# Kernel tuning notes

Measured on AMD Instinct MI355X. Metric: run time of the kernel, lower is better.

The kernel has to match this reference:

```python
import jax, jax.numpy as jnp
import numpy as np

N_NODES = 100000
N_EDGES = 600000
IN_DIM = 128
HID = 128
OUT_DIM = 64
N_LAYERS = 3


def setup_inputs() -> dict:
    key = jax.random.key(0)
    ks = jax.random.split(key, 8)
    x = jax.random.normal(ks[0], (N_NODES, IN_DIM), dtype=jnp.float32)
    edge_index = jax.random.randint(ks[1], (2, N_EDGES), 0, N_NODES, dtype=jnp.int64)
    s = 1.0 / np.sqrt(HID)
    W_in = jax.random.normal(ks[2], (HID, IN_DIM), dtype=jnp.float32) * s
    b_in = jax.random.normal(ks[3], (HID,), dtype=jnp.float32) * s
    W_convs = jax.random.normal(ks[4], (N_LAYERS, HID, HID), dtype=jnp.float32) * s
    b_convs = jax.random.normal(ks[5], (N_LAYERS, HID), dtype=jnp.float32) * s
    W_out = jax.random.normal(ks[6], (OUT_DIM, (N_LAYERS + 1) * HID), dtype=jnp.float32) * s
    b_out = jax.random.normal(ks[7], (OUT_DIM,), dtype=jnp.float32) * s
    return {"x": x, "edge_index": edge_index, "W_in": W_in, "b_in": b_in,
            "W_convs": W_convs, "b_convs": b_convs, "W_out": W_out, "b_out": b_out}


def reference(x, edge_index, W_in, b_in, W_convs, b_convs, W_out, b_out):
    src, dst = edge_index[0], edge_index[1]
    n = x.shape[0]
    # input projection: [N, in] -> [N, H]
    h = x @ W_in.T + b_in
    hidden_states = [h]
    for i in range(W_convs.shape[0]):
        # GINConv (eps=0): nn(x + sum of neighbor messages), messages src->dst
        agg = jax.ops.segment_sum(h[src], dst, num_segments=n)
        h = (h + agg) @ W_convs[i].T + b_convs[i]
        hidden_states.append(h)
    cat = jnp.concatenate(hidden_states, axis=1)  # [N, (L+1)*H]
    out = cat @ W_out.T + b_out  # [N, OUT]
    return jax.nn.softmax(out, axis=-1)
```

## Files before the change

### kernel.cpp

```cpp
#include <hip/hip_runtime.h>
#include <hip/hip_bf16.h>
#include <hip/hip_fp16.h>

#define GN 100000
#define GE 600000
#define SCAN_NBLK 98
#define ALD 132

typedef __bf16    bf16x8 __attribute__((ext_vector_type(8)));
typedef __bf16    bf16x4 __attribute__((ext_vector_type(4)));
typedef _Float16  f16x8  __attribute__((ext_vector_type(8)));
typedef float     f32x4  __attribute__((ext_vector_type(4)));

__global__ __launch_bounds__(256) void convert_w(
    const float* __restrict__ Win, const float* __restrict__ Wc,
    const float* __restrict__ Wout,
    __bf16* __restrict__ hi, __bf16* __restrict__ lo)
{
    const int i = blockIdx.x * 256 + threadIdx.x;
    if (i >= 98304) return;
    float v;
    if (i < 16384)      v = Win[i];
    else if (i < 65536) v = Wc[i - 16384];
    else                v = Wout[i - 65536];
    const __bf16 h = (__bf16)v;
    hi[i] = h;
    lo[i] = (__bf16)(v - (float)h);
}

__device__ __forceinline__ void gather8_f16(
    const uint* __restrict__ Hw,
    const int* __restrict__ row_start,
    const int* __restrict__ deg,
    const int* __restrict__ csr,
    const int row0, const int wave, const int lane,
    float* __restrict__ Acc)
{
    float2 acc8[8];
    int start8[8], deg8[8];
    int maxd = 0;
#pragma unroll
    for (int r = 0; r < 8; ++r) {
        acc8[r] = make_float2(0.f, 0.f);
        const int v = row0 + wave * 8 + r;
        start8[r] = row_start[v];
        deg8[r]   = deg[v];
        maxd = max(maxd, deg8[r]);
    }

    for (int b = 0; b < maxd; b += 64) {
        int idx8[8];
#pragma unroll
        for (int r = 0; r < 8; ++r) {
            const int off = max(min(b + lane, deg8[r] - 1), 0);
            idx8[r] = min(max(csr[start8[r] + off], 0), GN - 1);
        }
        const int wend = min(maxd - b, 64);
        for (int c = 0; c < wend; c += 8) {
            uint t[8][8];
#pragma unroll
            for (int cc = 0; cc < 8; ++cc)
#pragma unroll
                for (int r = 0; r < 8; ++r)
                    t[cc][r] = Hw[(size_t)__shfl(idx8[r], c + cc) * 64 + lane];
#pragma unroll
            for (int cc = 0; cc < 8; ++cc) {
                const int k = b + c + cc;
#pragma unroll
                for (int r = 0; r < 8; ++r) {
                    union { uint u; _Float16 h[2]; } cv;
                    cv.u = (k < deg8[r]) ? t[cc][r] : 0u;
                    acc8[r].x += (float)cv.h[0];
                    acc8[r].y += (float)cv.h[1];
                }
            }
        }
    }

    const int j = lane * 2;
#pragma unroll
    for (int r = 0; r < 8; ++r) {
        float* a = &Acc[(wave * 8 + r) * ALD + j];
        a[0] += acc8[r].x;
        a[1] += acc8[r].y;
    }
}

template<bool GATHER>
__global__ __launch_bounds__(256, 3) void gin_layer(
    const float* __restrict__ H, int ldH,
    const _Float16* __restrict__ HfIn,
    const int* __restrict__ row_start,
    const int* __restrict__ deg,
    const int* __restrict__ csr,
    const __bf16* __restrict__ Whi,
    const __bf16* __restrict__ Wlo,
    const float* __restrict__ bias,
    float* __restrict__ C, int ldC,
    _Float16* __restrict__ HfOut)
{
    __shared__ float Acc[32 * ALD];

    const int tid  = threadIdx.x;
    const int wave = tid >> 6;
    const int lane = tid & 63;
    const int row0 = blockIdx.x * 32;
    const int wn   = wave * 32;
    const int quad = lane >> 4;
    const int l15  = lane & 15;

    {
        const int sr = wave * 8 + (lane >> 5) ;
        float4 sv[4];
#pragma unroll
        for (int p = 0; p < 4; ++p) {
            const int r = wave * 8 + p * 2 + (lane >> 5);
            sv[p] = *(const float4*)(H + (size_t)(row0 + r) * ldH + (lane & 31) * 4);
        }
#pragma unroll
        for (int p = 0; p < 4; ++p) {
            const int r = wave * 8 + p * 2 + (lane >> 5);
            *(float4*)&Acc[r * ALD + (lane & 31) * 4] = sv[p];
        }
        (void)sr;
    }
    if (GATHER)
        gather8_f16((const uint*)HfIn, row_start, deg, csr, row0, wave, lane, Acc);
    __syncthreads();

    f32x4 acc[2][2];
#pragma unroll
    for (int i = 0; i < 2; ++i)
#pragma unroll
        for (int j = 0; j < 2; ++j) acc[i][j] = (f32x4)(0.0f);

    bf16x8 whA[2], wlA[2], whB[2], wlB[2];
#pragma unroll
    for (int nt = 0; nt < 2; ++nt) {
        const int n = wn + nt * 16 + l15;
        whA[nt] = *(const bf16x8*)(Whi + (size_t)n * 128 + quad * 8);
        wlA[nt] = *(const bf16x8*)(Wlo + (size_t)n * 128 + quad * 8);
    }

#pragma unroll
    for (int ks = 0; ks < 4; ++ks) {
        const int kt = ks * 32 + quad * 8;
        if (ks < 3) {
            const int kn = kt + 32;
#pragma unroll
            for (int nt = 0; nt < 2; ++nt) {
                const int n = wn + nt * 16 + l15;
                whB[nt] = *(const bf16x8*)(Whi + (size_t)n * 128 + kn);
                wlB[nt] = *(const bf16x8*)(Wlo + (size_t)n * 128 + kn);
            }
        }
        bf16x8 ahi[2], alo[2];
#pragma unroll
        for (int mt = 0; mt < 2; ++mt) {
            const float* ap = &Acc[(mt * 16 + l15) * ALD + kt];
            const f32x4 p = *(const f32x4*)ap;
            const f32x4 q = *(const f32x4*)(ap + 4);
#pragma unroll
            for (int e = 0; e < 4; ++e) {
                const __bf16 hp = (__bf16)p[e];
                const __bf16 hq = (__bf16)q[e];
                ahi[mt][e]     = hp;
                ahi[mt][e + 4] = hq;
                alo[mt][e]     = (__bf16)(p[e] - (float)hp);
                alo[mt][e + 4] = (__bf16)(q[e] - (float)hq);
            }
        }
#pragma unroll
        for (int mt = 0; mt < 2; ++mt)
#pragma unroll
            for (int nt = 0; nt < 2; ++nt) {
                acc[mt][nt] = __builtin_amdgcn_mfma_f32_16x16x32_bf16(
                    ahi[mt], whA[nt], acc[mt][nt], 0, 0, 0);
                acc[mt][nt] = __builtin_amdgcn_mfma_f32_16x16x32_bf16(
                    ahi[mt], wlA[nt], acc[mt][nt], 0, 0, 0);
                acc[mt][nt] = __builtin_amdgcn_mfma_f32_16x16x32_bf16(
                    alo[mt], whA[nt], acc[mt][nt], 0, 0, 0);
            }
        if (ks < 3) {
#pragma unroll
            for (int nt = 0; nt < 2; ++nt) {
                whA[nt] = whB[nt];
                wlA[nt] = wlB[nt];
            }
        }
    }
    __syncthreads();

#pragma unroll
    for (int nt = 0; nt < 2; ++nt) {
        const int col = wn + nt * 16 + l15;
        const float b = bias[col];
#pragma unroll
        for (int mt = 0; mt < 2; ++mt)
#pragma unroll
            for (int r4 = 0; r4 < 4; ++r4)
                Acc[(mt * 16 + quad * 4 + r4) * ALD + col] = acc[mt][nt][r4] + b;
    }
    __syncthreads();
#pragma unroll
    for (int p = 0; p < 4; ++p) {
        const int q  = tid + p * 256;
        const int r  = q >> 5;
        const int c4 = (q & 31) * 4;
        *(float4*)(C + (size_t)(row0 + r) * ldC + c4) = *(const float4*)&Acc[r * ALD + c4];
    }
#pragma unroll
    for (int p = 0; p < 2; ++p) {
        const int q = tid + p * 256;
        const int r = q >> 4;
        const int g = (q & 15) * 8;
        const float4 a = *(const float4*)&Acc[r * ALD + g];
        const float4 b = *(const float4*)&Acc[r * ALD + g + 4];
        f16x8 o = {(_Float16)a.x, (_Float16)a.y, (_Float16)a.z, (_Float16)a.w,
                   (_Float16)b.x, (_Float16)b.y, (_Float16)b.z, (_Float16)b.w};
        *(f16x8*)&HfOut[(size_t)(row0 + r) * 128 + g] = o;
    }
}

__global__ __launch_bounds__(256, 3) void gin_final(
    const float* __restrict__ cat3,
    const _Float16* __restrict__ HfIn,
    const int* __restrict__ row_start,
    const int* __restrict__ deg,
    const int* __restrict__ csr,
    const __bf16* __restrict__ Whi3,
    const __bf16* __restrict__ Wlo3,
    const float* __restrict__ b3,
    const __bf16* __restrict__ WhiO,
    const __bf16* __restrict__ WloO,
    const float* __restrict__ bO,
    float* __restrict__ out)
{
    constexpr int CLD = 68;

    __shared__ float Smem[32 * ALD];
    float* const Acc = Smem;
    float* const Cst = Smem;

    const int tid  = threadIdx.x;
    const int wave = tid >> 6;
    const int lane = tid & 63;
    const int row0 = blockIdx.x * 32;
    const int quad = lane >> 4;
    const int l15  = lane & 15;

    {
        float4 sv[4];
#pragma unroll
        for (int p = 0; p < 4; ++p) {
            const int r = wave * 8 + p * 2 + (lane >> 5);
            sv[p] = *(const float4*)(cat3 + (size_t)(row0 + r) * 384 + 256 + (lane & 31) * 4);
        }
#pragma unroll
        for (int p = 0; p < 4; ++p) {
            const int r = wave * 8 + p * 2 + (lane >> 5);
            *(float4*)&Acc[r * ALD + (lane & 31) * 4] = sv[p];
        }
    }
    gather8_f16((const uint*)HfIn, row_start, deg, csr, row0, wave, lane, Acc);
    __syncthreads();

    const int wn = wave * 32;
    f32x4 acc1[2][2];
#pragma unroll
    for (int i = 0; i < 2; ++i)
#pragma unroll
        for (int j = 0; j < 2; ++j) acc1[i][j] = (f32x4)(0.0f);

    {
        bf16x8 whA[2], wlA[2], whB[2], wlB[2];
#pragma unroll
        for (int nt = 0; nt < 2; ++nt) {
            const int n = wn + nt * 16 + l15;
            whA[nt] = *(const bf16x8*)(Whi3 + (size_t)n * 128 + quad * 8);
            wlA[nt] = *(const bf16x8*)(Wlo3 + (size_t)n * 128 + quad * 8);
        }
#pragma unroll
        for (int ks = 0; ks < 4; ++ks) {
            const int kt = ks * 32 + quad * 8;
            if (ks < 3) {
                const int kn = kt + 32;
#pragma unroll
                for (int nt = 0; nt < 2; ++nt) {
                    const int n = wn + nt * 16 + l15;
                    whB[nt] = *(const bf16x8*)(Whi3 + (size_t)n * 128 + kn);
                    wlB[nt] = *(const bf16x8*)(Wlo3 + (size_t)n * 128 + kn);
                }
            }
            bf16x8 ahi[2], alo[2];
#pragma unroll
            for (int mt = 0; mt < 2; ++mt) {
                const float* ap = &Acc[(mt * 16 + l15) * ALD + kt];
                const f32x4 p = *(const f32x4*)ap;
                const f32x4 q = *(const f32x4*)(ap + 4);
#pragma unroll
                for (int e = 0; e < 4; ++e) {
                    const __bf16 hp = (__bf16)p[e];
                    const __bf16 hq = (__bf16)q[e];
                    ahi[mt][e]     = hp;
                    ahi[mt][e + 4] = hq;
                    alo[mt][e]     = (__bf16)(p[e] - (float)hp);
                    alo[mt][e + 4] = (__bf16)(q[e] - (float)hq);
                }
            }
#pragma unroll
            for (int mt = 0; mt < 2; ++mt)
#pragma unroll
                for (int nt = 0; nt < 2; ++nt) {
                    acc1[mt][nt] = __builtin_amdgcn_mfma_f32_16x16x32_bf16(
                        ahi[mt], whA[nt], acc1[mt][nt], 0, 0, 0);
                    acc1[mt][nt] = __builtin_amdgcn_mfma_f32_16x16x32_bf16(
                        ahi[mt], wlA[nt], acc1[mt][nt], 0, 0, 0);
                    acc1[mt][nt] = __builtin_amdgcn_mfma_f32_16x16x32_bf16(
                        alo[mt], whA[nt], acc1[mt][nt], 0, 0, 0);
                }
            if (ks < 3) {
#pragma unroll
                for (int nt = 0; nt < 2; ++nt) {
                    whA[nt] = whB[nt];
                    wlA[nt] = wlB[nt];
                }
            }
        }
    }
    __syncthreads();

#pragma unroll
    for (int nt = 0; nt < 2; ++nt) {
        const int col = wn + nt * 16 + l15;
        const float b = b3[col];
#pragma unroll
        for (int mt = 0; mt < 2; ++mt)
#pragma unroll
            for (int r4 = 0; r4 < 4; ++r4)
                Acc[(mt * 16 + quad * 4 + r4) * ALD + col] = acc1[mt][nt][r4] + b;
    }
    __syncthreads();

    const int wk  = wave & 1;
    const int wn2 = (wave >> 1) * 32;
    f32x4 acc2[2][2];
#pragma unroll
    for (int i = 0; i < 2; ++i)
#pragma unroll
        for (int j = 0; j < 2; ++j) acc2[i][j] = (f32x4)(0.0f);

    f32x4 pA[2], qA[2], pB[2], qB[2];
    bf16x8 whA[2], wlA[2], whB[2], wlB[2];

    {
        const int kg = wk * 256 + quad * 8;
#pragma unroll
        for (int mt = 0; mt < 2; ++mt) {
            const int row = mt * 16 + l15;
            const float* ap = cat3 + (size_t)(row0 + row) * 384 + kg;
            pA[mt] = *(const f32x4*)ap;
            qA[mt] = *(const f32x4*)(ap + 4);
        }
#pragma unroll
        for (int nt = 0; nt < 2; ++nt) {
            const int n = wn2 + nt * 16 + l15;
            whA[nt] = *(const bf16x8*)(WhiO + (size_t)n * 512 + kg);
            wlA[nt] = *(const bf16x8*)(WloO + (size_t)n * 512 + kg);
        }
    }

#pragma unroll
    for (int ks = 0; ks < 8; ++ks) {
        if (ks < 7) {
            const int kg = wk * 256 + (ks + 1) * 32 + quad * 8;
#pragma unroll
            for (int mt = 0; mt < 2; ++mt) {
                const int row = mt * 16 + l15;
                if (kg < 384) {
                    const float* ap = cat3 + (size_t)(row0 + row) * 384 + kg;
                    pB[mt] = *(const f32x4*)ap;
                    qB[mt] = *(const f32x4*)(ap + 4);
                } else {
                    const float* ap = &Acc[row * ALD + (kg - 384)];
                    pB[mt] = *(const f32x4*)ap;
                    qB[mt] = *(const f32x4*)(ap + 4);
                }
            }
#pragma unroll
            for (int nt = 0; nt < 2; ++nt) {
                const int n = wn2 + nt * 16 + l15;
                whB[nt] = *(const bf16x8*)(WhiO + (size_t)n * 512 + kg);
                wlB[nt] = *(const bf16x8*)(WloO + (size_t)n * 512 + kg);
            }
        }
        bf16x8 ahi[2], alo[2];
#pragma unroll
        for (int mt = 0; mt < 2; ++mt) {
#pragma unroll
            for (int e = 0; e < 4; ++e) {
                const __bf16 hp = (__bf16)pA[mt][e];
                const __bf16 hq = (__bf16)qA[mt][e];
                ahi[mt][e]     = hp;
                ahi[mt][e + 4] = hq;
                alo[mt][e]     = (__bf16)(pA[mt][e] - (float)hp);
                alo[mt][e + 4] = (__bf16)(qA[mt][e] - (float)hq);
            }
        }
#pragma unroll
        for (int mt = 0; mt < 2; ++mt)
#pragma unroll
            for (int nt = 0; nt < 2; ++nt) {
                acc2[mt][nt] = __builtin_amdgcn_mfma_f32_16x16x32_bf16(
                    ahi[mt], whA[nt], acc2[mt][nt], 0, 0, 0);
                acc2[mt][nt] = __builtin_amdgcn_mfma_f32_16x16x32_bf16(
                    ahi[mt], wlA[nt], acc2[mt][nt], 0, 0, 0);
                acc2[mt][nt] = __builtin_amdgcn_mfma_f32_16x16x32_bf16(
                    alo[mt], whA[nt], acc2[mt][nt], 0, 0, 0);
            }
        if (ks < 7) {
#pragma unroll
            for (int mt = 0; mt < 2; ++mt) { pA[mt] = pB[mt]; qA[mt] = qB[mt]; }
#pragma unroll
            for (int nt = 0; nt < 2; ++nt) { whA[nt] = whB[nt]; wlA[nt] = wlB[nt]; }
        }
    }

    __syncthreads();

    if (wk == 1) {
#pragma unroll
        for (int nt = 0; nt < 2; ++nt)
#pragma unroll
            for (int mt = 0; mt < 2; ++mt)
#pragma unroll
                for (int r4 = 0; r4 < 4; ++r4)
                    Cst[(mt * 16 + quad * 4 + r4) * CLD + wn2 + nt * 16 + l15]
                        = acc2[mt][nt][r4];
    }
    __syncthreads();
    if (wk == 0) {
#pragma unroll
        for (int nt = 0; nt < 2; ++nt) {
            const int col = wn2 + nt * 16 + l15;
            const float b = bO[col];
#pragma unroll
            for (int mt = 0; mt < 2; ++mt)
#pragma unroll
                for (int r4 = 0; r4 < 4; ++r4) {
                    const int idx = (mt * 16 + quad * 4 + r4) * CLD + col;
                    Cst[idx] = Cst[idx] + acc2[mt][nt][r4] + b;
                }
        }
    }
    __syncthreads();

    for (int i = 0; i < 8; ++i) {
        const int r = wave * 8 + i;
        const float v = Cst[r * CLD + lane];
        float m = v;
#pragma unroll
        for (int off = 32; off > 0; off >>= 1) m = fmaxf(m, __shfl_xor(m, off));
        const float e = __expf(v - m);
        float s = e;
#pragma unroll
        for (int off = 32; off > 0; off >>= 1) s += __shfl_xor(s, off);
        out[(size_t)(row0 + r) * 64 + lane] = e / s;
    }
}

__global__ __launch_bounds__(256) void count_deg(const int* __restrict__ dst,
                                                 int* __restrict__ deg)
{
    const int e = blockIdx.x * 256 + threadIdx.x;
    if (e < GE) atomicAdd(&deg[dst[e]], 1);
}

__global__ __launch_bounds__(256) void scan_pass1(const int* __restrict__ deg,
                                                  int* __restrict__ excl,
                                                  int* __restrict__ blockSums)
{
    __shared__ int s[256];
    const int t = threadIdx.x;
    const int base = blockIdx.x * 1024 + t * 4;

    int4 v = make_int4(0, 0, 0, 0);
    if (base + 3 < GN) {
        v = *(const int4*)(deg + base);
    } else {
        if (base + 0 < GN) v.x = deg[base + 0];
        if (base + 1 < GN) v.y = deg[base + 1];
        if (base + 2 < GN) v.z = deg[base + 2];
        if (base + 3 < GN) v.w = deg[base + 3];
    }
    const int mysum = v.x + v.y + v.z + v.w;
    s[t] = mysum;
    __syncthreads();
    for (int off = 1; off < 256; off <<= 1) {
        const int val = (t >= off) ? s[t - off] : 0;
        __syncthreads();
        s[t] += val;
        __syncthreads();
    }
    int4 o;
    o.x = s[t] - mysum;
    o.y = o.x + v.x;
    o.z = o.y + v.y;
    o.w = o.z + v.z;
    if (base + 3 < GN) {
        *(int4*)(excl + base) = o;
    } else {
        if (base + 0 < GN) excl[base + 0] = o.x;
        if (base + 1 < GN) excl[base + 1] = o.y;
        if (base + 2 < GN) excl[base + 2] = o.z;
        if (base + 3 < GN) excl[base + 3] = o.w;
    }
    if (t == 255) blockSums[blockIdx.x] = s[255];
}

__global__ __launch_bounds__(128) void scan_pass2(const int* __restrict__ blockSums,
                                                  int* __restrict__ blockOffs, int n)
{
    __shared__ int s[128];
    const int t = threadIdx.x;
    const int v = (t < n) ? blockSums[t] : 0;
    s[t] = v;
    __syncthreads();
    for (int off = 1; off < 128; off <<= 1) {
        const int val = (t >= off) ? s[t - off] : 0;
        __syncthreads();
        s[t] += val;
        __syncthreads();
    }
    if (t < n) blockOffs[t] = s[t] - v;
}

__global__ __launch_bounds__(256) void scan_pass3(int* __restrict__ excl,
                                                  const int* __restrict__ blockOffs,
                                                  int* __restrict__ cursor)
{
    const int i = blockIdx.x * 256 + threadIdx.x;
    if (i >= GN) return;
    const int v = excl[i] + blockOffs[i >> 10];
    excl[i]   = v;
    cursor[i] = v;
}

__global__ __launch_bounds__(256) void fill_csr(const int* __restrict__ src,
                                                const int* __restrict__ dst,
                                                int* __restrict__ cursor,
                                                int* __restrict__ csr)
{
    const int e = blockIdx.x * 256 + threadIdx.x;
    if (e >= GE) return;
    const int pos = atomicAdd(&cursor[dst[e]], 1);
    csr[pos] = src[e];
}

extern "C" void kernel_launch(void* const* d_in, const int* in_sizes, int n_in,
                              void* d_out, int out_size, void* d_ws, size_t ws_size,
                              hipStream_t stream)
{
    const float* x       = (const float*)d_in[0];
    const int*   src     = (const int*)d_in[1];
    const int*   dst     = ((const int*)d_in[1]) + GE;
    const float* W_in    = (const float*)d_in[2];
    const float* b_in    = (const float*)d_in[3];
    const float* W_convs = (const float*)d_in[4];
    const float* b_convs = (const float*)d_in[5];
    const float* W_out   = (const float*)d_in[6];
    const float* b_out   = (const float*)d_in[7];
    float*       out     = (float*)d_out;

    float*    cat3 = (float*)d_ws;
    _Float16* Hf0  = (_Float16*)(cat3 + (size_t)GN * 384);
    _Float16* Hf1  = Hf0 + (size_t)GN * 128;
    int*      deg       = (int*)(Hf1 + (size_t)GN * 128);
    int*      row_start = deg + GN;
    int*      cursor    = row_start + GN;
    int*      blockSums = cursor + GN;
    int*      blockOffs = blockSums + 128;
    int*      csr       = blockOffs + 128;
    __bf16*   Whi       = (__bf16*)(csr + GE);
    __bf16*   Wlo       = Whi + 98304;

    const dim3 blk(256);
    const dim3 gblk(256);
    const int edge_blocks  = (GE + 255) / 256;
    const int node_blocks  = (GN + 255) / 256;
    const int layer_blocks = GN / 32;

    hipMemsetAsync(deg, 0, GN * sizeof(int), stream);
    count_deg<<<edge_blocks, blk, 0, stream>>>(dst, deg);
    scan_pass1<<<SCAN_NBLK, blk, 0, stream>>>(deg, row_start, blockSums);
    scan_pass2<<<1, 128, 0, stream>>>(blockSums, blockOffs, SCAN_NBLK);
    scan_pass3<<<node_blocks, blk, 0, stream>>>(row_start, blockOffs, cursor);
    fill_csr<<<edge_blocks, blk, 0, stream>>>(src, dst, cursor, csr);

    convert_w<<<(98304 + 255) / 256, blk, 0, stream>>>(W_in, W_convs, W_out, Whi, Wlo);

    gin_layer<false><<<layer_blocks, gblk, 0, stream>>>(
        x, 128, nullptr, nullptr, nullptr, nullptr,
        Whi, Wlo, b_in, cat3, 384, Hf0);

    gin_layer<true><<<layer_blocks, gblk, 0, stream>>>(
        cat3, 384, Hf0, row_start, deg, csr,
        Whi + 16384, Wlo + 16384, b_convs, cat3 + 128, 384, Hf1);
    gin_layer<true><<<layer_blocks, gblk, 0, stream>>>(
        cat3 + 128, 384, Hf1, row_start, deg, csr,
        Whi + 32768, Wlo + 32768, b_convs + 128, cat3 + 256, 384, Hf0);

    gin_final<<<layer_blocks, gblk, 0, stream>>>(
        cat3, Hf0, row_start, deg, csr,
        Whi + 49152, Wlo + 49152, b_convs + 256,
        Whi + 65536, Wlo + 65536, b_out, out);
}
```

Measured before the change: 473.1 us.

## Split neighbor gather into a standalone per-row kernel writing fp32 aggregates

Moves the fused in-GEMM neighbor aggregation out into a separate gather kernel, with one wave per destination row and high occupancy. It writes a float32 aggregate buffer that the layer GEMM kernels add to H when staging into LDS. The aim is to stop the gather's latency-bound, register-heavy loop from limiting the GEMM kernel's occupancy, and to avoid padding every row in a wave to the group's maximum degree. The cost is three extra launches plus writing and re-reading a 51 MB fp32 buffer per layer.

```diff
diff --git a/kernel.cpp b/kernel.cpp
--- a/kernel.cpp
+++ b/kernel.cpp
@@ -28,71 +28,51 @@
     lo[i] = (__bf16)(v - (float)h);
 }
 
-__device__ __forceinline__ void gather8_f16(
+__global__ __launch_bounds__(256, 8) void gather_rows(
     const uint* __restrict__ Hw,
     const int* __restrict__ row_start,
     const int* __restrict__ deg,
     const int* __restrict__ csr,
-    const int row0, const int wave, const int lane,
-    float* __restrict__ Acc)
-{
-    float2 acc8[8];
-    int start8[8], deg8[8];
-    int maxd = 0;
-#pragma unroll
-    for (int r = 0; r < 8; ++r) {
-        acc8[r] = make_float2(0.f, 0.f);
-        const int v = row0 + wave * 8 + r;
-        start8[r] = row_start[v];
-        deg8[r]   = deg[v];
-        maxd = max(maxd, deg8[r]);
-    }
-
-    for (int b = 0; b < maxd; b += 64) {
-        int idx8[8];
-#pragma unroll
-        for (int r = 0; r < 8; ++r) {
-            const int off = max(min(b + lane, deg8[r] - 1), 0);
-            idx8[r] = min(max(csr[start8[r] + off], 0), GN - 1);
-        }
-        const int wend = min(maxd - b, 64);
-        for (int c = 0; c < wend; c += 8) {
-            uint t[8][8];
-#pragma unroll
-            for (int cc = 0; cc < 8; ++cc)
-#pragma unroll
-                for (int r = 0; r < 8; ++r)
-                    t[cc][r] = Hw[(size_t)__shfl(idx8[r], c + cc) * 64 + lane];
-#pragma unroll
-            for (int cc = 0; cc < 8; ++cc) {
-                const int k = b + c + cc;
-#pragma unroll
-                for (int r = 0; r < 8; ++r) {
-                    union { uint u; _Float16 h[2]; } cv;
-                    cv.u = (k < deg8[r]) ? t[cc][r] : 0u;
-                    acc8[r].x += (float)cv.h[0];
-                    acc8[r].y += (float)cv.h[1];
-                }
-            }
-        }
-    }
-
-    const int j = lane * 2;
-#pragma unroll
-    for (int r = 0; r < 8; ++r) {
-        float* a = &Acc[(wave * 8 + r) * ALD + j];
-        a[0] += acc8[r].x;
-        a[1] += acc8[r].y;
-    }
-}
-
-template<bool GATHER>
+    float* __restrict__ Agg)
+{
+    const int wave = threadIdx.x >> 6;
+    const int lane = threadIdx.x & 63;
+    const int row  = blockIdx.x * 4 + wave;
+    if (row >= GN) return;
+
+    const int start = row_start[row];
+    const int dg    = deg[row];
+    float2 acc = make_float2(0.f, 0.f);
+
+    for (int b = 0; b < dg; b += 64) {
+        const int n = min(dg - b, 64);
+        const int idx = csr[start + min(b + lane, dg - 1)];
+        for (int k = 0; k < n; k += 8) {
+            uint t[8];
+#pragma unroll
+            for (int u = 0; u < 8; ++u) {
+                const int s = __shfl(idx, min(k + u, n - 1));
+                t[u] = Hw[(size_t)s * 64 + lane];
+            }
+            const int m = min(n - k, 8);
+#pragma unroll
+            for (int u = 0; u < 8; ++u) {
+                if (u < m) {
+                    union { uint uu; _Float16 h[2]; } cv;
+                    cv.uu = t[u];
+                    acc.x += (float)cv.h[0];
+                    acc.y += (float)cv.h[1];
+                }
+            }
+        }
+    }
+    *(float2*)&Agg[(size_t)row * 128 + lane * 2] = acc;
+}
+
+template<bool HASAGG>
 __global__ __launch_bounds__(256, 3) void gin_layer(
     const float* __restrict__ H, int ldH,
-    const _Float16* __restrict__ HfIn,
-    const int* __restrict__ row_start,
-    const int* __restrict__ deg,
-    const int* __restrict__ csr,
+    const float* __restrict__ Agg,
     const __bf16* __restrict__ Whi,
     const __bf16* __restrict__ Wlo,
     const float* __restrict__ bias,
@@ -110,22 +90,21 @@
     const int l15  = lane & 15;
 
     {
-        const int sr = wave * 8 + (lane >> 5) ;
-        float4 sv[4];
+        const int c = (lane & 31) * 4;
+        f32x4 sv[4];
 #pragma unroll
         for (int p = 0; p < 4; ++p) {
             const int r = wave * 8 + p * 2 + (lane >> 5);
-            sv[p] = *(const float4*)(H + (size_t)(row0 + r) * ldH + (lane & 31) * 4);
+            sv[p] = *(const f32x4*)(H + (size_t)(row0 + r) * ldH + c);
+            if (HASAGG)
+                sv[p] += *(const f32x4*)(Agg + (size_t)(row0 + r) * 128 + c);
         }
 #pragma unroll
         for (int p = 0; p < 4; ++p) {
             const int r = wave * 8 + p * 2 + (lane >> 5);
-            *(float4*)&Acc[r * ALD + (lane & 31) * 4] = sv[p];
-        }
-        (void)sr;
-    }
-    if (GATHER)
-        gather8_f16((const uint*)HfIn, row_start, deg, csr, row0, wave, lane, Acc);
+            *(f32x4*)&Acc[r * ALD + c] = sv[p];
+        }
+    }
     __syncthreads();
 
     f32x4 acc[2][2];
@@ -224,10 +203,7 @@
 
 __global__ __launch_bounds__(256, 3) void gin_final(
     const float* __restrict__ cat3,
-    const _Float16* __restrict__ HfIn,
-    const int* __restrict__ row_start,
-    const int* __restrict__ deg,
-    const int* __restrict__ csr,
+    const float* __restrict__ Agg,
     const __bf16* __restrict__ Whi3,
     const __bf16* __restrict__ Wlo3,
     const float* __restrict__ b3,
@@ -250,19 +226,20 @@
     const int l15  = lane & 15;
 
     {
-        float4 sv[4];
+        const int c = (lane & 31) * 4;
+        f32x4 sv[4];
 #pragma unroll
         for (int p = 0; p < 4; ++p) {
             const int r = wave * 8 + p * 2 + (lane >> 5);
-            sv[p] = *(const float4*)(cat3 + (size_t)(row0 + r) * 384 + 256 + (lane & 31) * 4);
+            sv[p] = *(const f32x4*)(cat3 + (size_t)(row0 + r) * 384 + 256 + c);
+            sv[p] += *(const f32x4*)(Agg + (size_t)(row0 + r) * 128 + c);
         }
 #pragma unroll
         for (int p = 0; p < 4; ++p) {
             const int r = wave * 8 + p * 2 + (lane >> 5);
-            *(float4*)&Acc[r * ALD + (lane & 31) * 4] = sv[p];
-        }
-    }
-    gather8_f16((const uint*)HfIn, row_start, deg, csr, row0, wave, lane, Acc);
+            *(f32x4*)&Acc[r * ALD + c] = sv[p];
+        }
+    }
     __syncthreads();
 
     const int wn = wave * 32;
@@ -573,9 +550,9 @@
     float*       out     = (float*)d_out;
 
     float*    cat3 = (float*)d_ws;
-    _Float16* Hf0  = (_Float16*)(cat3 + (size_t)GN * 384);
-    _Float16* Hf1  = Hf0 + (size_t)GN * 128;
-    int*      deg       = (int*)(Hf1 + (size_t)GN * 128);
+    _Float16* Hf   = (_Float16*)(cat3 + (size_t)GN * 384);
+    float*    Agg  = (float*)(Hf + (size_t)GN * 128);
+    int*      deg       = (int*)(Agg + (size_t)GN * 128);
     int*      row_start = deg + GN;
     int*      cursor    = row_start + GN;
     int*      blockSums = cursor + GN;
@@ -586,9 +563,10 @@
 
     const dim3 blk(256);
     const dim3 gblk(256);
-    const int edge_blocks  = (GE + 255) / 256;
-    const int node_blocks  = (GN + 255) / 256;
-    const int layer_blocks = GN / 32;
+    const int edge_blocks   = (GE + 255) / 256;
+    const int node_blocks   = (GN + 255) / 256;
+    const int layer_blocks  = GN / 32;
+    const int gather_blocks = (GN + 3) / 4;
 
     hipMemsetAsync(deg, 0, GN * sizeof(int), stream);
     count_deg<<<edge_blocks, blk, 0, stream>>>(dst, deg);
@@ -600,18 +578,22 @@
     convert_w<<<(98304 + 255) / 256, blk, 0, stream>>>(W_in, W_convs, W_out, Whi, Wlo);
 
     gin_layer<false><<<layer_blocks, gblk, 0, stream>>>(
-        x, 128, nullptr, nullptr, nullptr, nullptr,
-        Whi, Wlo, b_in, cat3, 384, Hf0);
-
+        x, 128, nullptr, Whi, Wlo, b_in, cat3, 384, Hf);
+
+    gather_rows<<<gather_blocks, gblk, 0, stream>>>(
+        (const uint*)Hf, row_start, deg, csr, Agg);
     gin_layer<true><<<layer_blocks, gblk, 0, stream>>>(
-        cat3, 384, Hf0, row_start, deg, csr,
-        Whi + 16384, Wlo + 16384, b_convs, cat3 + 128, 384, Hf1);
+        cat3, 384, Agg, Whi + 16384, Wlo + 16384, b_convs, cat3 + 128, 384, Hf);
+
+    gather_rows<<<gather_blocks, gblk, 0, stream>>>(
+        (const uint*)Hf, row_start, deg, csr, Agg);
     gin_layer<true><<<layer_blocks, gblk, 0, stream>>>(
-        cat3 + 128, 384, Hf1, row_start, deg, csr,
-        Whi + 32768, Wlo + 32768, b_convs + 128, cat3 + 256, 384, Hf0);
-
+        cat3 + 128, 384, Agg, Whi + 32768, Wlo + 32768, b_convs + 128,
+        cat3 + 256, 384, Hf);
+
+    gather_rows<<<gather_blocks, gblk, 0, stream>>>(
+        (const uint*)Hf, row_start, deg, csr, Agg);
     gin_final<<<layer_blocks, gblk, 0, stream>>>(
-        cat3, Hf0, row_start, deg, csr,
-        Whi + 49152, Wlo + 49152, b_convs + 256,
+        cat3, Agg, Whi + 49152, Wlo + 49152, b_convs + 256,
         Whi + 65536, Wlo + 65536, b_out, out);
 }
```

New measurement: 499.3 us. 5.5% more time.
